# Kernel optimization log

Hardware: AMD Instinct MI355X
Metric: run time of the kernel (lower is better)

The kernel has to match this reference:

```python
import jax, jax.numpy as jnp
import numpy as np

B, N, C, HEADS, P, H, W, TC, ITERS = 2, 4, 128, 8, 4, 96, 96, 64, 3
HD = C // HEADS  # 16
SHIFTS = [(0, 0), (-1, 0), (1, 0), (0, -1), (0, 1)]  # (dx, dy)


def conv1x1(x, w, b):
    # x [B,C,H,W], w [O,C], b [O]
    return jnp.einsum('bchw,oc->bohw', x, w) + b[None, :, None, None]


def grid_sample_bilinear(v, grid):
    # v [M,C,H,W]; grid [M,H,W,2] (x,y) in [-1,1]; align_corners=True, border padding
    M, Cc, Hh, Ww = v.shape
    ix = (grid[..., 0] + 1.0) * 0.5 * (Ww - 1)
    iy = (grid[..., 1] + 1.0) * 0.5 * (Hh - 1)
    x0 = jnp.floor(ix); y0 = jnp.floor(iy)
    wx = (ix - x0)[:, None]; wy = (iy - y0)[:, None]  # [M,1,H,W]
    x0i = jnp.clip(x0, 0, Ww - 1).astype(jnp.int32)
    x1i = jnp.clip(x0 + 1, 0, Ww - 1).astype(jnp.int32)
    y0i = jnp.clip(y0, 0, Hh - 1).astype(jnp.int32)
    y1i = jnp.clip(y0 + 1, 0, Hh - 1).astype(jnp.int32)
    vf = v.reshape(M, Cc, Hh * Ww)
    def gather(yi, xi):
        idx = (yi * Ww + xi).reshape(M, 1, Hh * Ww)
        return jnp.take_along_axis(vf, idx, axis=2).reshape(M, Cc, Hh, Ww)
    return (gather(y0i, x0i) * (1 - wx) * (1 - wy)
            + gather(y0i, x1i) * wx * (1 - wy)
            + gather(y1i, x0i) * (1 - wx) * wy
            + gather(y1i, x1i) * wx * wy)


def gru_cell(x, h, wih, whh, bih, bhh):
    gi = x @ wih.T + bih
    gh = h @ whh.T + bhh
    ir, iz, in_ = jnp.split(gi, 3, axis=-1)
    hr, hz, hn = jnp.split(gh, 3, axis=-1)
    r = jax.nn.sigmoid(ir + hr)
    z = jax.nn.sigmoid(iz + hz)
    n = jnp.tanh(in_ + r * hn)
    return (1.0 - z) * n + z * h


def _correlation_offsets(q, vn):
    # q, vn: [B,HEADS,HD,H,W]
    offset_vals = jnp.asarray(np.array(SHIFTS, dtype=np.float32))  # [5,2] (dx,dy)
    scores = []
    for dx, dy in SHIFTS:
        vs = jnp.roll(vn, shift=(dy, dx), axis=(-2, -1))
        if dy > 0: vs = vs.at[..., :dy, :].set(0.0)
        if dy < 0: vs = vs.at[..., dy:, :].set(0.0)
        if dx > 0: vs = vs.at[..., :, :dx].set(0.0)
        if dx < 0: vs = vs.at[..., :, dx:].set(0.0)
        scores.append((q * vs).sum(axis=2))  # [B,HEADS,H,W]
    best = jnp.argmax(jnp.stack(scores, axis=-1), axis=-1)  # [B,HEADS,H,W]
    bo = offset_vals[best]  # [B,HEADS,H,W,2]
    return jnp.stack([bo[..., 1] * (2.0 / W), bo[..., 0] * (2.0 / H)], axis=-1)


def _forward(query, values, rel_time, time_enc, qw, qb, vw, vb, dww, dwb, pww, pwb,
             wih, whh, bih, bhh, offw, offb, aw, ab, tw, tb, o1w, o1b, o2w, o2b, gate):
    q = conv1x1(query, qw, qb)
    v = conv1x1(values.reshape(B * N, C, H, W), vw, vb).reshape(B, N, C, H, W)
    q_heads = q.reshape(B, HEADS, HD, H, W)
    v_heads = v.reshape(B, N, HEADS, HD, H, W)

    # cnet: depthwise 7x7 -> GELU -> 1x1
    net = jax.lax.conv_general_dilated(query, dww, (1, 1), ((3, 3), (3, 3)),
                                       feature_group_count=C,
                                       dimension_numbers=('NCHW', 'OIHW', 'NCHW'))
    net = jax.nn.gelu(net + dwb[None, :, None, None], approximate=False)
    net = conv1x1(net, pww, pwb)
    net = net.reshape(B, HEADS, HD, H, W).transpose(0, 1, 3, 4, 2).reshape(-1, HD)

    nearest_idx = jnp.argmin(jnp.abs(rel_time), axis=1)  # [B]
    v_nearest = v_heads[jnp.arange(B), nearest_idx]  # [B,HEADS,HD,H,W]

    best_offset = _correlation_offsets(q_heads, v_nearest)  # [B,HEADS,H,W,2]
    curr_offsets = jnp.repeat(best_offset[:, :, :, :, None, :], P, axis=4)
    curr_attn = jnp.zeros((B, HEADS, H, W, N, P), jnp.float32)

    gy, gx = jnp.meshgrid(jnp.linspace(-1.0, 1.0, H), jnp.linspace(-1.0, 1.0, W), indexing='ij')
    base_grid = jnp.stack([gx, gy], axis=-1)  # [H,W,2]

    v_flat = v_nearest.reshape(B * HEADS, HD, H, W)
    for _ in range(ITERS):
        p0 = curr_offsets[..., 0, :]  # [B,HEADS,H,W,2]
        sg = jnp.clip((base_grid[None, None] + p0).reshape(B * HEADS, H, W, 2), -1.0, 1.0)
        sampled = grid_sample_bilinear(v_flat, sg)  # [B*HEADS,HD,H,W]
        sampled = sampled.transpose(0, 2, 3, 1).reshape(-1, HD)
        gru_in = jnp.concatenate([sampled, p0.reshape(-1, 2)], axis=-1)
        net = gru_cell(gru_in, net, wih, whh, bih, bhh)
        d_off = (net @ offw.T + offb).reshape(B, HEADS, H, W, P, 2)
        d_attn = (net @ aw.T + ab).reshape(B, HEADS, H, W, P)
        curr_offsets = curr_offsets + d_off
        curr_attn = curr_attn + d_attn[:, :, :, :, None, :]

    t_bias = (time_enc @ tw.T + tb).transpose(0, 2, 1).reshape(B, HEADS, 1, 1, N, 1)
    final_attn = curr_attn + t_bias
    attn_w = jax.nn.softmax(final_attn.reshape(B, HEADS, H, W, N * P), axis=-1)
    attn_w = attn_w.reshape(B, HEADS, H, W, N, P)

    # deformable sampling over all frames/points, vectorized via vmap
    grids = jnp.clip(base_grid[None, None, :, :, None, :] + curr_offsets, -1.0, 1.0)
    grids = grids.transpose(4, 0, 1, 2, 3, 5).reshape(P, B * HEADS, H, W, 2)
    v_all = v_heads.transpose(1, 0, 2, 3, 4, 5).reshape(N, B * HEADS, HD, H, W)
    samples = jax.vmap(lambda vn: jax.vmap(lambda g: grid_sample_bilinear(vn, g))(grids))(v_all)
    samples = samples.reshape(N, P, B, HEADS, HD, H, W)
    out = jnp.einsum('npbhcyx,bhyxnp->bhcyx', samples, attn_w).reshape(B, C, H, W)

    out = conv1x1(out, o1w, o1b)
    out = jax.nn.gelu(out, approximate=False)
    out = conv1x1(out, o2w, o2b) * jax.nn.sigmoid(gate)

    af = attn_w.reshape(B, HEADS, H, W, N * P)
    entropy = -(af * jnp.log(af + 1e-8)).sum(axis=-1).mean(axis=1, keepdims=True)
    max_ent = float(np.log(N * P))
    confidence = 1.0 - jnp.clip(entropy / (max_ent + 1e-8), 0.0, 1.0)
    return out, confidence, entropy


def setup_inputs():
    key = jax.random.key(0)
    ks = jax.random.split(key, 30)
    def nrm(k, shape, s=1.0):
        return jax.random.normal(k, shape, jnp.float32) * s
    s = 0.05
    return {
        'query': nrm(ks[0], (B, C, H, W)),
        'values': nrm(ks[1], (B, N, C, H, W)),
        'rel_time': nrm(ks[2], (B, N)),
        'time_enc': nrm(ks[3], (B, N, TC)),
        'qw': nrm(ks[4], (C, C), s), 'qb': nrm(ks[5], (C,), s),
        'vw': nrm(ks[6], (C, C), s), 'vb': nrm(ks[7], (C,), s),
        'dww': nrm(ks[8], (C, 1, 7, 7), s), 'dwb': nrm(ks[9], (C,), s),
        'pww': nrm(ks[10], (C, C), s), 'pwb': nrm(ks[11], (C,), s),
        'wih': nrm(ks[12], (3 * HD, HD + 2), s), 'whh': nrm(ks[13], (3 * HD, HD), s),
        'bih': nrm(ks[14], (3 * HD,), s), 'bhh': nrm(ks[15], (3 * HD,), s),
        'offw': nrm(ks[16], (P * 2, HD), s), 'offb': nrm(ks[17], (P * 2,), s),
        'aw': nrm(ks[18], (P, HD), s), 'ab': nrm(ks[19], (P,), s),
        'tw': nrm(ks[20], (HEADS, TC), s), 'tb': nrm(ks[21], (HEADS,), s),
        'o1w': nrm(ks[22], (C, C), s), 'o1b': nrm(ks[23], (C,), s),
        'o2w': nrm(ks[24], (C, C), s), 'o2b': nrm(ks[25], (C,), s),
        'gate': nrm(ks[26], (1, C, 1, 1), s),
    }


def reference(query, values, rel_time, time_enc, qw, qb, vw, vb, dww, dwb, pww, pwb,
              wih, whh, bih, bhh, offw, offb, aw, ab, tw, tb, o1w, o1b, o2w, o2b, gate):
    return _forward(query, values, rel_time, time_enc, qw, qb, vw, vb, dww, dwb, pww, pwb,
                    wih, whh, bih, bhh, offw, offb, aw, ab, tw, tb, o1w, o1b, o2w, o2b, gate)
```

## Files before the change

kernel.cpp:

```cpp
#include <hip/hip_runtime.h>
#include <hip/hip_bf16.h>

typedef unsigned short u16;
typedef unsigned int   u32;

constexpr int kHW = 9216;
constexpr int kM  = 147456;

__device__ __forceinline__ float gelu_f(float v){ return 0.5f*v*(1.0f+erff(v*0.70710678118654752f)); }
__device__ __forceinline__ float sigm_f(float v){ return 1.0f/(1.0f+expf(-v)); }
__device__ __forceinline__ u16 f2bf(float f){
  u32 x = __float_as_uint(f);
  return (u16)((x + 0x7fffu + ((x>>16)&1u)) >> 16);
}
__device__ __forceinline__ int nearest_n(const float* __restrict__ relt, int b){
  int nidx = 0; float bv = fabsf(relt[b*4]);
  for (int n = 1; n < 4; ++n){ float a = fabsf(relt[b*4+n]); if (a < bv){ bv=a; nidx=n; } }
  return nidx;
}

struct Bilin { int i00,i10,i01,i11; float w00,w10,w01,w11; };

__device__ __forceinline__ Bilin make_bilin(int x, int y, float ox, float oy){
  float gx = fmaf((float)x, 2.0f/95.0f, -1.0f);
  float gy = fmaf((float)y, 2.0f/95.0f, -1.0f);
  float sgx = fminf(fmaxf(gx+ox,-1.0f),1.0f);
  float sgy = fminf(fmaxf(gy+oy,-1.0f),1.0f);
  float ix = (sgx+1.0f)*0.5f*95.0f;
  float iy = (sgy+1.0f)*0.5f*95.0f;
  float x0f = floorf(ix), y0f = floorf(iy);
  float wx = ix-x0f, wy = iy-y0f;
  int x0 = min(max((int)x0f,0),95), y0 = min(max((int)y0f,0),95);
  int x1 = min(x0+1,95), y1 = min(y0+1,95);
  Bilin b;
  b.i00=(y0*96+x0)*16; b.i10=(y0*96+x1)*16; b.i01=(y1*96+x0)*16; b.i11=(y1*96+x1)*16;
  float iwx=1.0f-wx, iwy=1.0f-wy;
  b.w00=iwx*iwy; b.w10=wx*iwy; b.w01=iwx*wy; b.w11=wx*wy;
  return b;
}

__device__ __forceinline__ void sample16(const float* __restrict__ vp, const Bilin& bl, float* __restrict__ o){
  const float4* p00 = (const float4*)(vp + bl.i00);
  const float4* p10 = (const float4*)(vp + bl.i10);
  const float4* p01 = (const float4*)(vp + bl.i01);
  const float4* p11 = (const float4*)(vp + bl.i11);
  #pragma unroll
  for (int g = 0; g < 4; ++g){
    float4 a=p00[g], b=p10[g], c=p01[g], d=p11[g];
    o[g*4+0] = a.x*bl.w00 + b.x*bl.w10 + c.x*bl.w01 + d.x*bl.w11;
    o[g*4+1] = a.y*bl.w00 + b.y*bl.w10 + c.y*bl.w01 + d.y*bl.w11;
    o[g*4+2] = a.z*bl.w00 + b.z*bl.w10 + c.z*bl.w01 + d.z*bl.w11;
    o[g*4+3] = a.w*bl.w00 + b.w*bl.w10 + c.w*bl.w01 + d.w*bl.w11;
  }
}

__global__ __launch_bounds__(256) void prep_k(const float* __restrict__ qw, const float* __restrict__ vw,
    const float* __restrict__ pww, const float* __restrict__ o1w, const float* __restrict__ o2w,
    float* __restrict__ wt)
{
  const float* src = (blockIdx.y==0)?qw:(blockIdx.y==1)?vw:(blockIdx.y==2)?pww:(blockIdx.y==3)?o1w:o2w;
  float* d = wt + blockIdx.y*16384;
  int i = blockIdx.x*256 + threadIdx.x;
  int o = i & 127, c = i >> 7;
  d[i] = src[o*128 + c];
}

__global__ __launch_bounds__(256, 3) void gemm_qvp_k(
    const float* __restrict__ query, const float* __restrict__ values, const float* __restrict__ dwbuf,
    const float* __restrict__ wtb,
    const float* __restrict__ qb2, const float* __restrict__ vb2, const float* __restrict__ pwb2,
    float* __restrict__ qbuf, float* __restrict__ netb,
    float* __restrict__ vf32n, u16* __restrict__ vb16, const float* __restrict__ relt)
{
  __shared__ __align__(16) float a_s[16*132];
  __shared__ __align__(16) float b_s[16*132];
  const int tid = threadIdx.x;
  const int tx = tid & 15, ty = tid >> 4;
  const int iy = blockIdx.y;
  const float* inp; const float* wt; const float* bias; int img; int mode;
  if (iy < 2)       { inp = query;  wt = wtb;         bias = qb2;  img = iy;      mode = 0; }
  else if (iy < 10) { inp = values; wt = wtb + 16384; bias = vb2;  img = iy - 2;  mode = 1; }
  else              { inp = dwbuf;  wt = wtb + 32768; bias = pwb2; img = iy - 10; mode = 2; }
  const int px0 = blockIdx.x * 128;
  const int sr = tid >> 4;
  const int sc = (tid & 15) * 8;

  float acc[64];
  #pragma unroll
  for (int oj = 0; oj < 8; ++oj) {
    float bv = bias[tx*8+oj];
    #pragma unroll
    for (int pi = 0; pi < 8; ++pi) acc[pi*8+oj] = bv;
  }

  for (int kc = 0; kc < 8; ++kc) {
    const int k0 = kc*16;
    { const float4* g = (const float4*)(wt + (k0+sr)*128 + sc);
      float4 v0 = g[0], v1 = g[1];
      *(float4*)&b_s[sr*132+sc] = v0; *(float4*)&b_s[sr*132+sc+4] = v1; }
    { const float4* g = (const float4*)(inp + (size_t)(img*128 + k0 + sr)*kHW + px0 + sc);
      float4 v0 = g[0], v1 = g[1];
      *(float4*)&a_s[sr*132+sc] = v0; *(float4*)&a_s[sr*132+sc+4] = v1; }
    __syncthreads();
    #pragma unroll
    for (int k = 0; k < 16; ++k) {
      float4 b0 = *(const float4*)&b_s[k*132 + tx*8];
      float4 b1 = *(const float4*)&b_s[k*132 + tx*8 + 4];
      float4 a0 = *(const float4*)&a_s[k*132 + ty*8];
      float4 a1 = *(const float4*)&a_s[k*132 + ty*8 + 4];
      float av[8] = {a0.x,a0.y,a0.z,a0.w,a1.x,a1.y,a1.z,a1.w};
      float bv[8] = {b0.x,b0.y,b0.z,b0.w,b1.x,b1.y,b1.z,b1.w};
      #pragma unroll
      for (int pi = 0; pi < 8; ++pi)
        #pragma unroll
        for (int oj = 0; oj < 8; ++oj)
          acc[pi*8+oj] = fmaf(av[pi], bv[oj], acc[pi*8+oj]);
    }
    __syncthreads();
  }

  const int head = tx >> 1, hd0 = (tx & 1)*8;
  if (mode == 1) {
    const int b = img >> 2, n = img & 3;
    const int nidx = nearest_n(relt, b);
    #pragma unroll
    for (int pi = 0; pi < 8; ++pi) {
      const int px = px0 + ty*8 + pi;
      u16* d16 = vb16 + ((size_t)(img*8 + head)*kHW + px)*16 + hd0;
      uint4 packed;
      packed.x = (u32)f2bf(acc[pi*8+0]) | ((u32)f2bf(acc[pi*8+1])<<16);
      packed.y = (u32)f2bf(acc[pi*8+2]) | ((u32)f2bf(acc[pi*8+3])<<16);
      packed.z = (u32)f2bf(acc[pi*8+4]) | ((u32)f2bf(acc[pi*8+5])<<16);
      packed.w = (u32)f2bf(acc[pi*8+6]) | ((u32)f2bf(acc[pi*8+7])<<16);
      *(uint4*)d16 = packed;
      if (n == nidx) {
        float* dst = vf32n + ((size_t)(b*8 + head)*kHW + px)*16 + hd0;
        float4 t0 = {acc[pi*8+0],acc[pi*8+1],acc[pi*8+2],acc[pi*8+3]};
        float4 t1 = {acc[pi*8+4],acc[pi*8+5],acc[pi*8+6],acc[pi*8+7]};
        *(float4*)dst = t0; *(float4*)(dst+4) = t1;
      }
    }
  } else {
    float* outf = (mode == 0) ? qbuf : netb;
    #pragma unroll
    for (int pi = 0; pi < 8; ++pi) {
      const int px = px0 + ty*8 + pi;
      float* dst = outf + ((size_t)(img*8 + head)*kHW + px)*16 + hd0;
      float4 t0 = {acc[pi*8+0],acc[pi*8+1],acc[pi*8+2],acc[pi*8+3]};
      float4 t1 = {acc[pi*8+4],acc[pi*8+5],acc[pi*8+6],acc[pi*8+7]};
      *(float4*)dst = t0; *(float4*)(dst+4) = t1;
    }
  }
}

__global__ __launch_bounds__(256) void o1o2_k(const u16* __restrict__ oat,
    const float* __restrict__ wt1, const float* __restrict__ o1b,
    const float* __restrict__ wt2, const float* __restrict__ o2b,
    const float* __restrict__ gate, float* __restrict__ out)
{
  __shared__ __align__(16) float a_s[16*132];
  __shared__ __align__(16) float b_s[16*132];
  __shared__ __align__(16) float mid[128*132];
  const int tid = threadIdx.x;
  const int tx = tid & 15, ty = tid >> 4;
  const int img = blockIdx.y;
  const int px0 = blockIdx.x * 128;
  const int sr = tid >> 4;
  const int sc = (tid & 15) * 8;

  float acc[64];
  #pragma unroll
  for (int oj = 0; oj < 8; ++oj) {
    float bv = o1b[tx*8+oj];
    #pragma unroll
    for (int pi = 0; pi < 8; ++pi) acc[pi*8+oj] = bv;
  }
  for (int kc = 0; kc < 8; ++kc) {
    const int k0 = kc*16;
    { const float4* g = (const float4*)(wt1 + (k0+sr)*128 + sc);
      float4 v0 = g[0], v1 = g[1];
      *(float4*)&b_s[sr*132+sc] = v0; *(float4*)&b_s[sr*132+sc+4] = v1; }
    { const int px = tid >> 1, hd0 = (tid & 1)*8;
      uint4 raw = *(const uint4*)(oat + ((size_t)(img*8 + kc)*kHW + px0 + px)*16 + hd0);
      u32 w[4] = {raw.x, raw.y, raw.z, raw.w};
      #pragma unroll
      for (int gi = 0; gi < 4; ++gi) {
        a_s[(hd0+gi*2+0)*132+px] = __uint_as_float(w[gi]<<16);
        a_s[(hd0+gi*2+1)*132+px] = __uint_as_float(w[gi]&0xffff0000u);
      }
    }
    __syncthreads();
    #pragma unroll
    for (int k = 0; k < 16; ++k) {
      float4 b0 = *(const float4*)&b_s[k*132 + tx*8];
      float4 b1 = *(const float4*)&b_s[k*132 + tx*8 + 4];
      float4 a0 = *(const float4*)&a_s[k*132 + ty*8];
      float4 a1 = *(const float4*)&a_s[k*132 + ty*8 + 4];
      float av[8] = {a0.x,a0.y,a0.z,a0.w,a1.x,a1.y,a1.z,a1.w};
      float bv[8] = {b0.x,b0.y,b0.z,b0.w,b1.x,b1.y,b1.z,b1.w};
      #pragma unroll
      for (int pi = 0; pi < 8; ++pi)
        #pragma unroll
        for (int oj = 0; oj < 8; ++oj)
          acc[pi*8+oj] = fmaf(av[pi], bv[oj], acc[pi*8+oj]);
    }
    __syncthreads();
  }
  #pragma unroll
  for (int oj = 0; oj < 8; ++oj)
    #pragma unroll
    for (int pi = 0; pi < 8; ++pi)
      mid[(tx*8+oj)*132 + ty*8+pi] = gelu_f(acc[pi*8+oj]);
  __syncthreads();

  #pragma unroll
  for (int oj = 0; oj < 8; ++oj) {
    float bv = o2b[tx*8+oj];
    #pragma unroll
    for (int pi = 0; pi < 8; ++pi) acc[pi*8+oj] = bv;
  }
  for (int kc = 0; kc < 8; ++kc) {
    const int k0 = kc*16;
    { const float4* g = (const float4*)(wt2 + (k0+sr)*128 + sc);
      float4 v0 = g[0], v1 = g[1];
      *(float4*)&b_s[sr*132+sc] = v0; *(float4*)&b_s[sr*132+sc+4] = v1; }
    __syncthreads();
    #pragma unroll
    for (int k = 0; k < 16; ++k) {
      float4 b0 = *(const float4*)&b_s[k*132 + tx*8];
      float4 b1 = *(const float4*)&b_s[k*132 + tx*8 + 4];
      float4 a0 = *(const float4*)&mid[(k0+k)*132 + ty*8];
      float4 a1 = *(const float4*)&mid[(k0+k)*132 + ty*8 + 4];
      float av[8] = {a0.x,a0.y,a0.z,a0.w,a1.x,a1.y,a1.z,a1.w};
      float bv[8] = {b0.x,b0.y,b0.z,b0.w,b1.x,b1.y,b1.z,b1.w};
      #pragma unroll
      for (int pi = 0; pi < 8; ++pi)
        #pragma unroll
        for (int oj = 0; oj < 8; ++oj)
          acc[pi*8+oj] = fmaf(av[pi], bv[oj], acc[pi*8+oj]);
    }
    __syncthreads();
  }
  #pragma unroll
  for (int oj = 0; oj < 8; ++oj) {
    const int o = tx*8 + oj;
    float* dst = out + (size_t)(img*128 + o)*kHW + px0 + ty*8;
    float sg = sigm_f(gate[o]);
    float v[8];
    #pragma unroll
    for (int pi = 0; pi < 8; ++pi) v[pi] = acc[pi*8+oj] * sg;
    float4 t0 = {v[0],v[1],v[2],v[3]};
    float4 t1 = {v[4],v[5],v[6],v[7]};
    *(float4*)dst = t0; *(float4*)(dst+4) = t1;
  }
}

__global__ __launch_bounds__(256) void dw_k(const float* __restrict__ q, const float* __restrict__ dww,
    const float* __restrict__ dwb, float* __restrict__ outf)
{
  int idx = blockIdx.x*256 + threadIdx.x;
  int px = idx % kHW;
  int bc = idx / kHW;
  int c = bc & 127;
  int x = px % 96, y = px / 96;
  float s = dwb[c];
  const float* qb = q + (size_t)bc*kHW;
  #pragma unroll
  for (int ky = 0; ky < 7; ++ky) {
    int yy = y + ky - 3;
    if (yy < 0 || yy > 95) continue;
    #pragma unroll
    for (int kx = 0; kx < 7; ++kx) {
      int xx = x + kx - 3;
      if (xx < 0 || xx > 95) continue;
      s = fmaf(qb[yy*96+xx], dww[c*49 + ky*7 + kx], s);
    }
  }
  outf[idx] = gelu_f(s);
}

__global__ void tb_k(const float* __restrict__ te, const float* __restrict__ tw,
                     const float* __restrict__ tbias, float* __restrict__ tbb)
{
  int i = threadIdx.x;
  if (i >= 64) return;
  int b = i >> 5, h = (i >> 2) & 7, n = i & 3;
  float s = tbias[h];
  for (int tc = 0; tc < 64; ++tc) s = fmaf(te[(b*4+n)*64 + tc], tw[h*64+tc], s);
  tbb[(b*8+h)*4 + n] = s;
}

__global__ __launch_bounds__(256) void fused_k(
    const float* __restrict__ qb, const float* __restrict__ vf32, const u16* __restrict__ vb16,
    const float* __restrict__ netb, const float* __restrict__ relt,
    const float* __restrict__ wih, const float* __restrict__ whh,
    const float* __restrict__ bihp, const float* __restrict__ bhhp,
    const float* __restrict__ offw, const float* __restrict__ offbp,
    const float* __restrict__ aw, const float* __restrict__ abp,
    const float* __restrict__ tbb,
    u16* __restrict__ outattn16, float* __restrict__ entb)
{
  __shared__ __align__(16) float s_wih[48*20];
  __shared__ __align__(16) float s_whh[48*16];
  __shared__ __align__(16) float s_offw[8*16];
  __shared__ __align__(16) float s_aw[4*16];
  __shared__ float s_bih[48], s_bhh[48], s_offb[8], s_ab[4];
  const int tid = threadIdx.x;
  for (int i = tid; i < 960; i += 256){ int g = i/20, k = i%20; s_wih[i] = (k<18)? wih[g*18+k] : 0.0f; }
  for (int i = tid; i < 768; i += 256) s_whh[i] = whh[i];
  if (tid < 128) s_offw[tid] = offw[tid];
  if (tid < 64)  s_aw[tid]  = aw[tid];
  if (tid < 48){ s_bih[tid] = bihp[tid]; s_bhh[tid] = bhhp[tid]; }
  if (tid < 8)   s_offb[tid] = offbp[tid];
  if (tid < 4)   s_ab[tid]  = abp[tid];

  const int vblk = (blockIdx.x & 7)*72 + (blockIdx.x >> 3);
  const int item = vblk*256 + tid;
  const int yx = item % kHW; const int bh = item / kHW;
  const int b = bh >> 3, head = bh & 7;
  const int x = yx % 96, y = yx / 96;
  const float* vp = vf32 + (size_t)(b*8 + head)*kM;

  float off_[8], attn_[4];
  {
    float qv[16];
    { const float4* q4 = (const float4*)(qb + (size_t)bh*kM + yx*16);
      #pragma unroll
      for (int g = 0; g < 4; ++g){ float4 t = q4[g]; qv[g*4]=t.x; qv[g*4+1]=t.y; qv[g*4+2]=t.z; qv[g*4+3]=t.w; } }
    const int sdx[5] = {0,-1,1,0,0};
    const int sdy[5] = {0,0,0,-1,1};
    float4 tv[5][4]; bool valid[5];
    #pragma unroll
    for (int s5 = 0; s5 < 5; ++s5) {
      int sy = y - sdy[s5], sx = x - sdx[s5];
      valid[s5] = (sy >= 0 && sy < 96 && sx >= 0 && sx < 96);
      int syc = min(max(sy,0),95), sxc = min(max(sx,0),95);
      const float4* tp = (const float4*)(vp + (syc*96+sxc)*16);
      tv[s5][0] = tp[0]; tv[s5][1] = tp[1]; tv[s5][2] = tp[2]; tv[s5][3] = tp[3];
    }
    double bsc = 0.0; int best = 0;
    #pragma unroll
    for (int s5 = 0; s5 < 5; ++s5) {
      double sc = 0.0;
      if (valid[s5]) {
        const float* tp = (const float*)&tv[s5][0];
        #pragma unroll
        for (int hd = 0; hd < 16; ++hd) sc += (double)qv[hd]*(double)tp[hd];
      }
      if (s5 == 0) { bsc = sc; best = 0; }
      else if (sc > bsc) { bsc = sc; best = s5; }
    }
    const float STEP = 2.0f/96.0f;
    float ox = 0.f, oy = 0.f;
    if (best == 3) ox = -STEP; else if (best == 4) ox = STEP;
    if (best == 1) oy = -STEP; else if (best == 2) oy = STEP;
    #pragma unroll
    for (int p = 0; p < 4; ++p) { off_[2*p] = ox; off_[2*p+1] = oy; attn_[p] = 0.0f; }
  }

  float h[16];
  { const float4* n4 = (const float4*)(netb + (size_t)item*16);
    #pragma unroll
    for (int g = 0; g < 4; ++g){ float4 t = n4[g]; h[g*4]=t.x; h[g*4+1]=t.y; h[g*4+2]=t.z; h[g*4+3]=t.w; } }

  __syncthreads();

  for (int it = 0; it < 3; ++it) {
    const float p0x = off_[0];
    const float p0y = off_[1];
    Bilin bl = make_bilin(x, y, p0x, p0y);
    float xv[20];
    sample16(vp, bl, xv);
    xv[16] = p0x; xv[17] = p0y; xv[18] = 0.f; xv[19] = 0.f;

    float hn[16];
    #pragma unroll 2
    for (int j = 0; j < 16; ++j) {
      float g0 = s_bih[j], g1 = s_bih[16+j], g2 = s_bih[32+j];
      const float4* w0r = (const float4*)&s_wih[j*20];
      const float4* w1r = (const float4*)&s_wih[(16+j)*20];
      const float4* w2r = (const float4*)&s_wih[(32+j)*20];
      #pragma unroll
      for (int q4 = 0; q4 < 5; ++q4) {
        float4 w0 = w0r[q4], w1 = w1r[q4], w2 = w2r[q4];
        float a0 = xv[q4*4+0], a1 = xv[q4*4+1], a2 = xv[q4*4+2], a3 = xv[q4*4+3];
        g0 = fmaf(a0,w0.x,g0); g0 = fmaf(a1,w0.y,g0); g0 = fmaf(a2,w0.z,g0); g0 = fmaf(a3,w0.w,g0);
        g1 = fmaf(a0,w1.x,g1); g1 = fmaf(a1,w1.y,g1); g1 = fmaf(a2,w1.z,g1); g1 = fmaf(a3,w1.w,g1);
        g2 = fmaf(a0,w2.x,g2); g2 = fmaf(a1,w2.y,g2); g2 = fmaf(a2,w2.z,g2); g2 = fmaf(a3,w2.w,g2);
      }
      float t0 = s_bhh[j], t1 = s_bhh[16+j], t2 = s_bhh[32+j];
      const float4* h0r = (const float4*)&s_whh[j*16];
      const float4* h1r = (const float4*)&s_whh[(16+j)*16];
      const float4* h2r = (const float4*)&s_whh[(32+j)*16];
      #pragma unroll
      for (int q4 = 0; q4 < 4; ++q4) {
        float4 w0 = h0r[q4], w1 = h1r[q4], w2 = h2r[q4];
        float a0 = h[q4*4+0], a1 = h[q4*4+1], a2 = h[q4*4+2], a3 = h[q4*4+3];
        t0 = fmaf(a0,w0.x,t0); t0 = fmaf(a1,w0.y,t0); t0 = fmaf(a2,w0.z,t0); t0 = fmaf(a3,w0.w,t0);
        t1 = fmaf(a0,w1.x,t1); t1 = fmaf(a1,w1.y,t1); t1 = fmaf(a2,w1.z,t1); t1 = fmaf(a3,w1.w,t1);
        t2 = fmaf(a0,w2.x,t2); t2 = fmaf(a1,w2.y,t2); t2 = fmaf(a2,w2.z,t2); t2 = fmaf(a3,w2.w,t2);
      }
      float r = sigm_f(g0 + t0);
      float z = sigm_f(g1 + t1);
      float nn = tanhf(fmaf(r, t2, g2));
      hn[j] = fmaf(z, h[j], (1.0f - z)*nn);
    }
    #pragma unroll
    for (int j = 0; j < 16; ++j) h[j] = hn[j];

    #pragma unroll
    for (int d = 0; d < 8; ++d) {
      const float4* wr = (const float4*)&s_offw[d*16];
      float s = s_offb[d];
      #pragma unroll
      for (int q4 = 0; q4 < 4; ++q4) {
        float4 w4 = wr[q4];
        s = fmaf(h[q4*4+0], w4.x, s); s = fmaf(h[q4*4+1], w4.y, s);
        s = fmaf(h[q4*4+2], w4.z, s); s = fmaf(h[q4*4+3], w4.w, s);
      }
      off_[d] += s;
    }
    #pragma unroll
    for (int p = 0; p < 4; ++p) {
      const float4* wr = (const float4*)&s_aw[p*16];
      float s = s_ab[p];
      #pragma unroll
      for (int q4 = 0; q4 < 4; ++q4) {
        float4 w4 = wr[q4];
        s = fmaf(h[q4*4+0], w4.x, s); s = fmaf(h[q4*4+1], w4.y, s);
        s = fmaf(h[q4*4+2], w4.z, s); s = fmaf(h[q4*4+3], w4.w, s);
      }
      attn_[p] += s;
    }
  }

  float lg[16];
  #pragma unroll
  for (int n = 0; n < 4; ++n) {
    float tv2 = tbb[(b*8+head)*4 + n];
    #pragma unroll
    for (int p = 0; p < 4; ++p) lg[n*4+p] = attn_[p] + tv2;
  }
  float mx = lg[0];
  #pragma unroll
  for (int i = 1; i < 16; ++i) mx = fmaxf(mx, lg[i]);
  float es = 0.f;
  #pragma unroll
  for (int i = 0; i < 16; ++i){ lg[i] = expf(lg[i]-mx); es += lg[i]; }
  float inv = 1.0f/es;
  float ent = 0.f;
  #pragma unroll
  for (int i = 0; i < 16; ++i){ lg[i] *= inv; ent -= lg[i]*logf(lg[i] + 1e-8f); }
  entb[item] = ent;

  float acc[16];
  #pragma unroll
  for (int j = 0; j < 16; ++j) acc[j] = 0.f;
  #pragma unroll
  for (int p = 0; p < 4; ++p) {
    Bilin bl = make_bilin(x, y, off_[2*p], off_[2*p+1]);
    uint4 raw[4][8];
    #pragma unroll
    for (int n = 0; n < 4; ++n) {
      const u16* vpn = vb16 + (size_t)((b*4+n)*8 + head)*kM;
      raw[n][0] = *(const uint4*)(vpn + bl.i00); raw[n][1] = *(const uint4*)(vpn + bl.i00 + 8);
      raw[n][2] = *(const uint4*)(vpn + bl.i10); raw[n][3] = *(const uint4*)(vpn + bl.i10 + 8);
      raw[n][4] = *(const uint4*)(vpn + bl.i01); raw[n][5] = *(const uint4*)(vpn + bl.i01 + 8);
      raw[n][6] = *(const uint4*)(vpn + bl.i11); raw[n][7] = *(const uint4*)(vpn + bl.i11 + 8);
    }
    #pragma unroll
    for (int n = 0; n < 4; ++n) {
      u32 aw2[8] = {raw[n][0].x,raw[n][0].y,raw[n][0].z,raw[n][0].w, raw[n][1].x,raw[n][1].y,raw[n][1].z,raw[n][1].w};
      u32 bw2[8] = {raw[n][2].x,raw[n][2].y,raw[n][2].z,raw[n][2].w, raw[n][3].x,raw[n][3].y,raw[n][3].z,raw[n][3].w};
      u32 cw2[8] = {raw[n][4].x,raw[n][4].y,raw[n][4].z,raw[n][4].w, raw[n][5].x,raw[n][5].y,raw[n][5].z,raw[n][5].w};
      u32 dw2[8] = {raw[n][6].x,raw[n][6].y,raw[n][6].z,raw[n][6].w, raw[n][7].x,raw[n][7].y,raw[n][7].z,raw[n][7].w};
      float wnp = lg[n*4+p];
      #pragma unroll
      for (int g = 0; g < 8; ++g){
        float alo = __uint_as_float(aw2[g]<<16), ahi = __uint_as_float(aw2[g]&0xffff0000u);
        float blo = __uint_as_float(bw2[g]<<16), bhi = __uint_as_float(bw2[g]&0xffff0000u);
        float clo = __uint_as_float(cw2[g]<<16), chi = __uint_as_float(cw2[g]&0xffff0000u);
        float dlo = __uint_as_float(dw2[g]<<16), dhi = __uint_as_float(dw2[g]&0xffff0000u);
        float s0 = alo*bl.w00 + blo*bl.w10 + clo*bl.w01 + dlo*bl.w11;
        float s1 = ahi*bl.w00 + bhi*bl.w10 + chi*bl.w01 + dhi*bl.w11;
        acc[g*2+0] = fmaf(wnp, s0, acc[g*2+0]);
        acc[g*2+1] = fmaf(wnp, s1, acc[g*2+1]);
      }
    }
  }
  uint4 pk0, pk1;
  pk0.x = (u32)f2bf(acc[0])  | ((u32)f2bf(acc[1])<<16);
  pk0.y = (u32)f2bf(acc[2])  | ((u32)f2bf(acc[3])<<16);
  pk0.z = (u32)f2bf(acc[4])  | ((u32)f2bf(acc[5])<<16);
  pk0.w = (u32)f2bf(acc[6])  | ((u32)f2bf(acc[7])<<16);
  pk1.x = (u32)f2bf(acc[8])  | ((u32)f2bf(acc[9])<<16);
  pk1.y = (u32)f2bf(acc[10]) | ((u32)f2bf(acc[11])<<16);
  pk1.z = (u32)f2bf(acc[12]) | ((u32)f2bf(acc[13])<<16);
  pk1.w = (u32)f2bf(acc[14]) | ((u32)f2bf(acc[15])<<16);
  *(uint4*)(outattn16 + (size_t)item*16)     = pk0;
  *(uint4*)(outattn16 + (size_t)item*16 + 8) = pk1;
}

__global__ __launch_bounds__(256) void ent_k(const float* __restrict__ entb, float* __restrict__ outf)
{
  int idx = blockIdx.x*256 + threadIdx.x;
  int b = idx / kHW, yx = idx % kHW;
  float s = 0.f;
  #pragma unroll
  for (int h8 = 0; h8 < 8; ++h8) s += entb[(b*8+h8)*kHW + yx];
  s *= 0.125f;
  float conf = 1.0f - fminf(fmaxf(s / (2.772588722239781f + 1e-8f), 0.0f), 1.0f);
  outf[2359296 + idx]         = conf;
  outf[2359296 + 18432 + idx] = s;
}

extern "C" void kernel_launch(void* const* d_in, const int* in_sizes, int n_in,
                              void* d_out, int out_size, void* d_ws, size_t ws_size,
                              hipStream_t stream)
{
  const float* query  = (const float*)d_in[0];
  const float* values = (const float*)d_in[1];
  const float* relt   = (const float*)d_in[2];
  const float* time_enc = (const float*)d_in[3];
  const float* qw  = (const float*)d_in[4];
  const float* qb  = (const float*)d_in[5];
  const float* vw  = (const float*)d_in[6];
  const float* vb  = (const float*)d_in[7];
  const float* dww = (const float*)d_in[8];
  const float* dwb = (const float*)d_in[9];
  const float* pww = (const float*)d_in[10];
  const float* pwb = (const float*)d_in[11];
  const float* wih = (const float*)d_in[12];
  const float* whh = (const float*)d_in[13];
  const float* bih = (const float*)d_in[14];
  const float* bhh = (const float*)d_in[15];
  const float* offw = (const float*)d_in[16];
  const float* offb = (const float*)d_in[17];
  const float* aw  = (const float*)d_in[18];
  const float* ab  = (const float*)d_in[19];
  const float* tw  = (const float*)d_in[20];
  const float* tb  = (const float*)d_in[21];
  const float* o1w = (const float*)d_in[22];
  const float* o1b = (const float*)d_in[23];
  const float* o2w = (const float*)d_in[24];
  const float* o2b = (const float*)d_in[25];
  const float* gate = (const float*)d_in[26];
  float* out = (float*)d_out;
  float* ws = (float*)d_ws;

  u16*   vb16   = (u16*)ws;
  float* vf32n  = ws + 4718592;
  float* qbuf   = ws + 7077888;
  float* netb   = ws + 9437184;
  float* dwbuf  = ws + 11796480;
  u16*   oat16  = (u16*)dwbuf;
  float* entbf  = ws + 14155776;
  float* tbbuf  = ws + 14303232;
  float* wtbuf  = ws + 14303360;
  if (ws_size < 14385280ull * 4ull) return;

  float* wt_o1 = wtbuf + 49152;
  float* wt_o2 = wtbuf + 65536;

  dim3 blk(256,1,1);
  prep_k<<<dim3(64,5,1), blk, 0, stream>>>(qw, vw, pww, o1w, o2w, wtbuf);
  dw_k<<<dim3(9216,1,1), blk, 0, stream>>>(query, dww, dwb, dwbuf);
  gemm_qvp_k<<<dim3(72,12,1), blk, 0, stream>>>(query, values, dwbuf, wtbuf,
                                                qb, vb, pwb, qbuf, netb, vf32n, vb16, relt);
  tb_k<<<dim3(1,1,1), dim3(64,1,1), 0, stream>>>(time_enc, tw, tb, tbbuf);
  fused_k<<<dim3(576,1,1), blk, 0, stream>>>(qbuf, vf32n, vb16, netb, relt,
                                             wih, whh, bih, bhh, offw, offb, aw, ab,
                                             tbbuf, oat16, entbf);
  ent_k<<<dim3(72,1,1), blk, 0, stream>>>(entbf, out);
  o1o2_k<<<dim3(72,2,1), blk, 0, stream>>>(oat16, wt_o1, o1b, wt_o2, o2b, gate, out);
}
```

Measured before the change: 434.8 us.

## Halve o1o2 pixel tile and read GRU weights directly from global memory

Measured after the change: 445.5 us. +2.5%, slower.

```diff
diff --git a/kernel.cpp b/kernel.cpp
--- a/kernel.cpp
+++ b/kernel.cpp
@@ -158,48 +158,44 @@
     const float* __restrict__ wt2, const float* __restrict__ o2b,
     const float* __restrict__ gate, float* __restrict__ out)
 {
-  __shared__ __align__(16) float a_s[16*132];
+  __shared__ __align__(16) float a_s[16*68];
   __shared__ __align__(16) float b_s[16*132];
-  __shared__ __align__(16) float mid[128*132];
+  __shared__ __align__(16) float mid[128*68];
   const int tid = threadIdx.x;
   const int tx = tid & 15, ty = tid >> 4;
   const int img = blockIdx.y;
-  const int px0 = blockIdx.x * 128;
+  const int px0 = blockIdx.x * 64;
   const int sr = tid >> 4;
   const int sc = (tid & 15) * 8;
 
-  float acc[64];
+  float acc[32];
   #pragma unroll
   for (int oj = 0; oj < 8; ++oj) {
     float bv = o1b[tx*8+oj];
     #pragma unroll
-    for (int pi = 0; pi < 8; ++pi) acc[pi*8+oj] = bv;
+    for (int pi = 0; pi < 4; ++pi) acc[pi*8+oj] = bv;
   }
   for (int kc = 0; kc < 8; ++kc) {
     const int k0 = kc*16;
     { const float4* g = (const float4*)(wt1 + (k0+sr)*128 + sc);
       float4 v0 = g[0], v1 = g[1];
       *(float4*)&b_s[sr*132+sc] = v0; *(float4*)&b_s[sr*132+sc+4] = v1; }
-    { const int px = tid >> 1, hd0 = (tid & 1)*8;
-      uint4 raw = *(const uint4*)(oat + ((size_t)(img*8 + kc)*kHW + px0 + px)*16 + hd0);
-      u32 w[4] = {raw.x, raw.y, raw.z, raw.w};
-      #pragma unroll
-      for (int gi = 0; gi < 4; ++gi) {
-        a_s[(hd0+gi*2+0)*132+px] = __uint_as_float(w[gi]<<16);
-        a_s[(hd0+gi*2+1)*132+px] = __uint_as_float(w[gi]&0xffff0000u);
-      }
-    }
+    { const int px = tid & 63, hd0 = (tid >> 6) * 4;
+      uint2 raw = *(const uint2*)(oat + ((size_t)(img*8 + kc)*kHW + px0 + px)*16 + hd0);
+      a_s[(hd0+0)*68+px] = __uint_as_float(raw.x<<16);
+      a_s[(hd0+1)*68+px] = __uint_as_float(raw.x&0xffff0000u);
+      a_s[(hd0+2)*68+px] = __uint_as_float(raw.y<<16);
+      a_s[(hd0+3)*68+px] = __uint_as_float(raw.y&0xffff0000u); }
     __syncthreads();
     #pragma unroll
     for (int k = 0; k < 16; ++k) {
       float4 b0 = *(const float4*)&b_s[k*132 + tx*8];
       float4 b1 = *(const float4*)&b_s[k*132 + tx*8 + 4];
-      float4 a0 = *(const float4*)&a_s[k*132 + ty*8];
-      float4 a1 = *(const float4*)&a_s[k*132 + ty*8 + 4];
-      float av[8] = {a0.x,a0.y,a0.z,a0.w,a1.x,a1.y,a1.z,a1.w};
+      float4 a0 = *(const float4*)&a_s[k*68 + ty*4];
+      float av[4] = {a0.x,a0.y,a0.z,a0.w};
       float bv[8] = {b0.x,b0.y,b0.z,b0.w,b1.x,b1.y,b1.z,b1.w};
       #pragma unroll
-      for (int pi = 0; pi < 8; ++pi)
+      for (int pi = 0; pi < 4; ++pi)
         #pragma unroll
         for (int oj = 0; oj < 8; ++oj)
           acc[pi*8+oj] = fmaf(av[pi], bv[oj], acc[pi*8+oj]);
@@ -209,15 +205,15 @@
   #pragma unroll
   for (int oj = 0; oj < 8; ++oj)
     #pragma unroll
-    for (int pi = 0; pi < 8; ++pi)
-      mid[(tx*8+oj)*132 + ty*8+pi] = gelu_f(acc[pi*8+oj]);
+    for (int pi = 0; pi < 4; ++pi)
+      mid[(tx*8+oj)*68 + ty*4+pi] = gelu_f(acc[pi*8+oj]);
   __syncthreads();
 
   #pragma unroll
   for (int oj = 0; oj < 8; ++oj) {
     float bv = o2b[tx*8+oj];
     #pragma unroll
-    for (int pi = 0; pi < 8; ++pi) acc[pi*8+oj] = bv;
+    for (int pi = 0; pi < 4; ++pi) acc[pi*8+oj] = bv;
   }
   for (int kc = 0; kc < 8; ++kc) {
     const int k0 = kc*16;
@@ -229,12 +225,11 @@
     for (int k = 0; k < 16; ++k) {
       float4 b0 = *(const float4*)&b_s[k*132 + tx*8];
       float4 b1 = *(const float4*)&b_s[k*132 + tx*8 + 4];
-      float4 a0 = *(const float4*)&mid[(k0+k)*132 + ty*8];
-      float4 a1 = *(const float4*)&mid[(k0+k)*132 + ty*8 + 4];
-      float av[8] = {a0.x,a0.y,a0.z,a0.w,a1.x,a1.y,a1.z,a1.w};
+      float4 a0 = *(const float4*)&mid[(k0+k)*68 + ty*4];
+      float av[4] = {a0.x,a0.y,a0.z,a0.w};
       float bv[8] = {b0.x,b0.y,b0.z,b0.w,b1.x,b1.y,b1.z,b1.w};
       #pragma unroll
-      for (int pi = 0; pi < 8; ++pi)
+      for (int pi = 0; pi < 4; ++pi)
         #pragma unroll
         for (int oj = 0; oj < 8; ++oj)
           acc[pi*8+oj] = fmaf(av[pi], bv[oj], acc[pi*8+oj]);
@@ -244,14 +239,10 @@
   #pragma unroll
   for (int oj = 0; oj < 8; ++oj) {
     const int o = tx*8 + oj;
-    float* dst = out + (size_t)(img*128 + o)*kHW + px0 + ty*8;
+    float* dst = out + (size_t)(img*128 + o)*kHW + px0 + ty*4;
     float sg = sigm_f(gate[o]);
-    float v[8];
-    #pragma unroll
-    for (int pi = 0; pi < 8; ++pi) v[pi] = acc[pi*8+oj] * sg;
-    float4 t0 = {v[0],v[1],v[2],v[3]};
-    float4 t1 = {v[4],v[5],v[6],v[7]};
-    *(float4*)dst = t0; *(float4*)(dst+4) = t1;
+    float4 t0 = {acc[0*8+oj]*sg, acc[1*8+oj]*sg, acc[2*8+oj]*sg, acc[3*8+oj]*sg};
+    *(float4*)dst = t0;
   }
 }
 
@@ -300,20 +291,7 @@
     const float* __restrict__ tbb,
     u16* __restrict__ outattn16, float* __restrict__ entb)
 {
-  __shared__ __align__(16) float s_wih[48*20];
-  __shared__ __align__(16) float s_whh[48*16];
-  __shared__ __align__(16) float s_offw[8*16];
-  __shared__ __align__(16) float s_aw[4*16];
-  __shared__ float s_bih[48], s_bhh[48], s_offb[8], s_ab[4];
   const int tid = threadIdx.x;
-  for (int i = tid; i < 960; i += 256){ int g = i/20, k = i%20; s_wih[i] = (k<18)? wih[g*18+k] : 0.0f; }
-  for (int i = tid; i < 768; i += 256) s_whh[i] = whh[i];
-  if (tid < 128) s_offw[tid] = offw[tid];
-  if (tid < 64)  s_aw[tid]  = aw[tid];
-  if (tid < 48){ s_bih[tid] = bihp[tid]; s_bhh[tid] = bhhp[tid]; }
-  if (tid < 8)   s_offb[tid] = offbp[tid];
-  if (tid < 4)   s_ab[tid]  = abp[tid];
-
   const int vblk = (blockIdx.x & 7)*72 + (blockIdx.x >> 3);
   const int item = vblk*256 + tid;
   const int yx = item % kHW; const int bh = item / kHW;
@@ -363,42 +341,38 @@
     #pragma unroll
     for (int g = 0; g < 4; ++g){ float4 t = n4[g]; h[g*4]=t.x; h[g*4+1]=t.y; h[g*4+2]=t.z; h[g*4+3]=t.w; } }
 
-  __syncthreads();
-
   for (int it = 0; it < 3; ++it) {
     const float p0x = off_[0];
     const float p0y = off_[1];
     Bilin bl = make_bilin(x, y, p0x, p0y);
-    float xv[20];
+    float xv[18];
     sample16(vp, bl, xv);
-    xv[16] = p0x; xv[17] = p0y; xv[18] = 0.f; xv[19] = 0.f;
+    xv[16] = p0x; xv[17] = p0y;
 
     float hn[16];
     #pragma unroll 2
     for (int j = 0; j < 16; ++j) {
-      float g0 = s_bih[j], g1 = s_bih[16+j], g2 = s_bih[32+j];
-      const float4* w0r = (const float4*)&s_wih[j*20];
-      const float4* w1r = (const float4*)&s_wih[(16+j)*20];
-      const float4* w2r = (const float4*)&s_wih[(32+j)*20];
-      #pragma unroll
-      for (int q4 = 0; q4 < 5; ++q4) {
-        float4 w0 = w0r[q4], w1 = w1r[q4], w2 = w2r[q4];
-        float a0 = xv[q4*4+0], a1 = xv[q4*4+1], a2 = xv[q4*4+2], a3 = xv[q4*4+3];
-        g0 = fmaf(a0,w0.x,g0); g0 = fmaf(a1,w0.y,g0); g0 = fmaf(a2,w0.z,g0); g0 = fmaf(a3,w0.w,g0);
-        g1 = fmaf(a0,w1.x,g1); g1 = fmaf(a1,w1.y,g1); g1 = fmaf(a2,w1.z,g1); g1 = fmaf(a3,w1.w,g1);
-        g2 = fmaf(a0,w2.x,g2); g2 = fmaf(a1,w2.y,g2); g2 = fmaf(a2,w2.z,g2); g2 = fmaf(a3,w2.w,g2);
+      float g0 = bihp[j], g1 = bihp[16+j], g2 = bihp[32+j];
+      const float* w0 = wih + j*18;
+      const float* w1 = wih + (16+j)*18;
+      const float* w2 = wih + (32+j)*18;
+      #pragma unroll
+      for (int k = 0; k < 18; ++k) {
+        float a = xv[k];
+        g0 = fmaf(a, w0[k], g0);
+        g1 = fmaf(a, w1[k], g1);
+        g2 = fmaf(a, w2[k], g2);
       }
-      float t0 = s_bhh[j], t1 = s_bhh[16+j], t2 = s_bhh[32+j];
-      const float4* h0r = (const float4*)&s_whh[j*16];
-      const float4* h1r = (const float4*)&s_whh[(16+j)*16];
-      const float4* h2r = (const float4*)&s_whh[(32+j)*16];
-      #pragma unroll
-      for (int q4 = 0; q4 < 4; ++q4) {
-        float4 w0 = h0r[q4], w1 = h1r[q4], w2 = h2r[q4];
-        float a0 = h[q4*4+0], a1 = h[q4*4+1], a2 = h[q4*4+2], a3 = h[q4*4+3];
-        t0 = fmaf(a0,w0.x,t0); t0 = fmaf(a1,w0.y,t0); t0 = fmaf(a2,w0.z,t0); t0 = fmaf(a3,w0.w,t0);
-        t1 = fmaf(a0,w1.x,t1); t1 = fmaf(a1,w1.y,t1); t1 = fmaf(a2,w1.z,t1); t1 = fmaf(a3,w1.w,t1);
-        t2 = fmaf(a0,w2.x,t2); t2 = fmaf(a1,w2.y,t2); t2 = fmaf(a2,w2.z,t2); t2 = fmaf(a3,w2.w,t2);
+      float t0 = bhhp[j], t1 = bhhp[16+j], t2 = bhhp[32+j];
+      const float* v0 = whh + j*16;
+      const float* v1 = whh + (16+j)*16;
+      const float* v2 = whh + (32+j)*16;
+      #pragma unroll
+      for (int k = 0; k < 16; ++k) {
+        float a = h[k];
+        t0 = fmaf(a, v0[k], t0);
+        t1 = fmaf(a, v1[k], t1);
+        t2 = fmaf(a, v2[k], t2);
       }
       float r = sigm_f(g0 + t0);
       float z = sigm_f(g1 + t1);
@@ -410,26 +384,18 @@
 
     #pragma unroll
     for (int d = 0; d < 8; ++d) {
-      const float4* wr = (const float4*)&s_offw[d*16];
-      float s = s_offb[d];
-      #pragma unroll
-      for (int q4 = 0; q4 < 4; ++q4) {
-        float4 w4 = wr[q4];
-        s = fmaf(h[q4*4+0], w4.x, s); s = fmaf(h[q4*4+1], w4.y, s);
-        s = fmaf(h[q4*4+2], w4.z, s); s = fmaf(h[q4*4+3], w4.w, s);
-      }
+      const float* wr = offw + d*16;
+      float s = offbp[d];
+      #pragma unroll
+      for (int k = 0; k < 16; ++k) s = fmaf(h[k], wr[k], s);
       off_[d] += s;
     }
     #pragma unroll
     for (int p = 0; p < 4; ++p) {
-      const float4* wr = (const float4*)&s_aw[p*16];
-      float s = s_ab[p];
-      #pragma unroll
-      for (int q4 = 0; q4 < 4; ++q4) {
-        float4 w4 = wr[q4];
-        s = fmaf(h[q4*4+0], w4.x, s); s = fmaf(h[q4*4+1], w4.y, s);
-        s = fmaf(h[q4*4+2], w4.z, s); s = fmaf(h[q4*4+3], w4.w, s);
-      }
+      const float* wr = aw + p*16;
+      float s = abp[p];
+      #pragma unroll
+      for (int k = 0; k < 16; ++k) s = fmaf(h[k], wr[k], s);
       attn_[p] += s;
     }
   }
@@ -572,5 +538,5 @@
                                              wih, whh, bih, bhh, offw, offb, aw, ab,
                                              tbbuf, oat16, entbf);
   ent_k<<<dim3(72,1,1), blk, 0, stream>>>(entbf, out);
-  o1o2_k<<<dim3(72,2,1), blk, 0, stream>>>(oat16, wt_o1, o1b, wt_o2, o2b, gate, out);
-}
+  o1o2_k<<<dim3(144,2,1), blk, 0, stream>>>(oat16, wt_o1, o1b, wt_o2, o2b, gate, out);
+}
```

## Merge small launches and shrink output-MLP tile to raise block count

Applied to the files above, without the earlier changes.

Result: faster. 423.6 us (-2.6%).

```diff
diff --git a/kernel.cpp b/kernel.cpp
--- a/kernel.cpp
+++ b/kernel.cpp
@@ -54,15 +54,49 @@
   }
 }
 
-__global__ __launch_bounds__(256) void prep_k(const float* __restrict__ qw, const float* __restrict__ vw,
-    const float* __restrict__ pww, const float* __restrict__ o1w, const float* __restrict__ o2w,
-    float* __restrict__ wt)
+__global__ __launch_bounds__(256) void pre_k(
+    const float* __restrict__ query, const float* __restrict__ dww, const float* __restrict__ dwb,
+    float* __restrict__ dwbuf,
+    const float* __restrict__ qw, const float* __restrict__ vw, const float* __restrict__ pww,
+    const float* __restrict__ o1w, const float* __restrict__ o2w, float* __restrict__ wt,
+    const float* __restrict__ te, const float* __restrict__ tw, const float* __restrict__ tbias,
+    float* __restrict__ tbb)
 {
-  const float* src = (blockIdx.y==0)?qw:(blockIdx.y==1)?vw:(blockIdx.y==2)?pww:(blockIdx.y==3)?o1w:o2w;
-  float* d = wt + blockIdx.y*16384;
-  int i = blockIdx.x*256 + threadIdx.x;
-  int o = i & 127, c = i >> 7;
-  d[i] = src[o*128 + c];
+  const int bid = blockIdx.x;
+  const int tid = threadIdx.x;
+  if (bid < 9216) {
+    int idx = bid*256 + tid;
+    int px = idx % kHW;
+    int bc = idx / kHW;
+    int c = bc & 127;
+    int x = px % 96, y = px / 96;
+    float s = dwb[c];
+    const float* qb = query + (size_t)bc*kHW;
+    #pragma unroll
+    for (int ky = 0; ky < 7; ++ky) {
+      int yy = y + ky - 3;
+      if (yy < 0 || yy > 95) continue;
+      #pragma unroll
+      for (int kx = 0; kx < 7; ++kx) {
+        int xx = x + kx - 3;
+        if (xx < 0 || xx > 95) continue;
+        s = fmaf(qb[yy*96+xx], dww[c*49 + ky*7 + kx], s);
+      }
+    }
+    dwbuf[idx] = gelu_f(s);
+  } else if (bid < 9536) {
+    int i = (bid - 9216)*256 + tid;
+    int m = i >> 14, r = i & 16383;
+    const float* src = (m==0)?qw:(m==1)?vw:(m==2)?pww:(m==3)?o1w:o2w;
+    int o = r & 127, c = r >> 7;
+    wt[m*16384 + r] = src[o*128 + c];
+  } else {
+    if (tid >= 64) return;
+    int b = tid >> 5, h = (tid >> 2) & 7, n = tid & 3;
+    float s = tbias[h];
+    for (int tc = 0; tc < 64; ++tc) s = fmaf(te[(b*4+n)*64 + tc], tw[h*64+tc], s);
+    tbb[(b*8+h)*4 + n] = s;
+  }
 }
 
 __global__ __launch_bounds__(256, 3) void gemm_qvp_k(
@@ -151,143 +185,6 @@
       *(float4*)dst = t0; *(float4*)(dst+4) = t1;
     }
   }
-}
-
-__global__ __launch_bounds__(256) void o1o2_k(const u16* __restrict__ oat,
-    const float* __restrict__ wt1, const float* __restrict__ o1b,
-    const float* __restrict__ wt2, const float* __restrict__ o2b,
-    const float* __restrict__ gate, float* __restrict__ out)
-{
-  __shared__ __align__(16) float a_s[16*132];
-  __shared__ __align__(16) float b_s[16*132];
-  __shared__ __align__(16) float mid[128*132];
-  const int tid = threadIdx.x;
-  const int tx = tid & 15, ty = tid >> 4;
-  const int img = blockIdx.y;
-  const int px0 = blockIdx.x * 128;
-  const int sr = tid >> 4;
-  const int sc = (tid & 15) * 8;
-
-  float acc[64];
-  #pragma unroll
-  for (int oj = 0; oj < 8; ++oj) {
-    float bv = o1b[tx*8+oj];
-    #pragma unroll
-    for (int pi = 0; pi < 8; ++pi) acc[pi*8+oj] = bv;
-  }
-  for (int kc = 0; kc < 8; ++kc) {
-    const int k0 = kc*16;
-    { const float4* g = (const float4*)(wt1 + (k0+sr)*128 + sc);
-      float4 v0 = g[0], v1 = g[1];
-      *(float4*)&b_s[sr*132+sc] = v0; *(float4*)&b_s[sr*132+sc+4] = v1; }
-    { const int px = tid >> 1, hd0 = (tid & 1)*8;
-      uint4 raw = *(const uint4*)(oat + ((size_t)(img*8 + kc)*kHW + px0 + px)*16 + hd0);
-      u32 w[4] = {raw.x, raw.y, raw.z, raw.w};
-      #pragma unroll
-      for (int gi = 0; gi < 4; ++gi) {
-        a_s[(hd0+gi*2+0)*132+px] = __uint_as_float(w[gi]<<16);
-        a_s[(hd0+gi*2+1)*132+px] = __uint_as_float(w[gi]&0xffff0000u);
-      }
-    }
-    __syncthreads();
-    #pragma unroll
-    for (int k = 0; k < 16; ++k) {
-      float4 b0 = *(const float4*)&b_s[k*132 + tx*8];
-      float4 b1 = *(const float4*)&b_s[k*132 + tx*8 + 4];
-      float4 a0 = *(const float4*)&a_s[k*132 + ty*8];
-      float4 a1 = *(const float4*)&a_s[k*132 + ty*8 + 4];
-      float av[8] = {a0.x,a0.y,a0.z,a0.w,a1.x,a1.y,a1.z,a1.w};
-      float bv[8] = {b0.x,b0.y,b0.z,b0.w,b1.x,b1.y,b1.z,b1.w};
-      #pragma unroll
-      for (int pi = 0; pi < 8; ++pi)
-        #pragma unroll
-        for (int oj = 0; oj < 8; ++oj)
-          acc[pi*8+oj] = fmaf(av[pi], bv[oj], acc[pi*8+oj]);
-    }
-    __syncthreads();
-  }
-  #pragma unroll
-  for (int oj = 0; oj < 8; ++oj)
-    #pragma unroll
-    for (int pi = 0; pi < 8; ++pi)
-      mid[(tx*8+oj)*132 + ty*8+pi] = gelu_f(acc[pi*8+oj]);
-  __syncthreads();
-
-  #pragma unroll
-  for (int oj = 0; oj < 8; ++oj) {
-    float bv = o2b[tx*8+oj];
-    #pragma unroll
-    for (int pi = 0; pi < 8; ++pi) acc[pi*8+oj] = bv;
-  }
-  for (int kc = 0; kc < 8; ++kc) {
-    const int k0 = kc*16;
-    { const float4* g = (const float4*)(wt2 + (k0+sr)*128 + sc);
-      float4 v0 = g[0], v1 = g[1];
-      *(float4*)&b_s[sr*132+sc] = v0; *(float4*)&b_s[sr*132+sc+4] = v1; }
-    __syncthreads();
-    #pragma unroll
-    for (int k = 0; k < 16; ++k) {
-      float4 b0 = *(const float4*)&b_s[k*132 + tx*8];
-      float4 b1 = *(const float4*)&b_s[k*132 + tx*8 + 4];
-      float4 a0 = *(const float4*)&mid[(k0+k)*132 + ty*8];
-      float4 a1 = *(const float4*)&mid[(k0+k)*132 + ty*8 + 4];
-      float av[8] = {a0.x,a0.y,a0.z,a0.w,a1.x,a1.y,a1.z,a1.w};
-      float bv[8] = {b0.x,b0.y,b0.z,b0.w,b1.x,b1.y,b1.z,b1.w};
-      #pragma unroll
-      for (int pi = 0; pi < 8; ++pi)
-        #pragma unroll
-        for (int oj = 0; oj < 8; ++oj)
-          acc[pi*8+oj] = fmaf(av[pi], bv[oj], acc[pi*8+oj]);
-    }
-    __syncthreads();
-  }
-  #pragma unroll
-  for (int oj = 0; oj < 8; ++oj) {
-    const int o = tx*8 + oj;
-    float* dst = out + (size_t)(img*128 + o)*kHW + px0 + ty*8;
-    float sg = sigm_f(gate[o]);
-    float v[8];
-    #pragma unroll
-    for (int pi = 0; pi < 8; ++pi) v[pi] = acc[pi*8+oj] * sg;
-    float4 t0 = {v[0],v[1],v[2],v[3]};
-    float4 t1 = {v[4],v[5],v[6],v[7]};
-    *(float4*)dst = t0; *(float4*)(dst+4) = t1;
-  }
-}
-
-__global__ __launch_bounds__(256) void dw_k(const float* __restrict__ q, const float* __restrict__ dww,
-    const float* __restrict__ dwb, float* __restrict__ outf)
-{
-  int idx = blockIdx.x*256 + threadIdx.x;
-  int px = idx % kHW;
-  int bc = idx / kHW;
-  int c = bc & 127;
-  int x = px % 96, y = px / 96;
-  float s = dwb[c];
-  const float* qb = q + (size_t)bc*kHW;
-  #pragma unroll
-  for (int ky = 0; ky < 7; ++ky) {
-    int yy = y + ky - 3;
-    if (yy < 0 || yy > 95) continue;
-    #pragma unroll
-    for (int kx = 0; kx < 7; ++kx) {
-      int xx = x + kx - 3;
-      if (xx < 0 || xx > 95) continue;
-      s = fmaf(qb[yy*96+xx], dww[c*49 + ky*7 + kx], s);
-    }
-  }
-  outf[idx] = gelu_f(s);
-}
-
-__global__ void tb_k(const float* __restrict__ te, const float* __restrict__ tw,
-                     const float* __restrict__ tbias, float* __restrict__ tbb)
-{
-  int i = threadIdx.x;
-  if (i >= 64) return;
-  int b = i >> 5, h = (i >> 2) & 7, n = i & 3;
-  float s = tbias[h];
-  for (int tc = 0; tc < 64; ++tc) s = fmaf(te[(b*4+n)*64 + tc], tw[h*64+tc], s);
-  tbb[(b*8+h)*4 + n] = s;
 }
 
 __global__ __launch_bounds__(256) void fused_k(
@@ -501,17 +398,110 @@
   *(uint4*)(outattn16 + (size_t)item*16 + 8) = pk1;
 }
 
-__global__ __launch_bounds__(256) void ent_k(const float* __restrict__ entb, float* __restrict__ outf)
+__global__ __launch_bounds__(256) void tail_k(const u16* __restrict__ oat,
+    const float* __restrict__ wt1, const float* __restrict__ o1b,
+    const float* __restrict__ wt2, const float* __restrict__ o2b,
+    const float* __restrict__ gate, const float* __restrict__ entb, float* __restrict__ out)
 {
-  int idx = blockIdx.x*256 + threadIdx.x;
-  int b = idx / kHW, yx = idx % kHW;
-  float s = 0.f;
-  #pragma unroll
-  for (int h8 = 0; h8 < 8; ++h8) s += entb[(b*8+h8)*kHW + yx];
-  s *= 0.125f;
-  float conf = 1.0f - fminf(fmaxf(s / (2.772588722239781f + 1e-8f), 0.0f), 1.0f);
-  outf[2359296 + idx]         = conf;
-  outf[2359296 + 18432 + idx] = s;
+  __shared__ __align__(16) float a_s[16*68];
+  __shared__ __align__(16) float b_s[16*132];
+  __shared__ __align__(16) float mid[128*68];
+  const int tid = threadIdx.x;
+  if (blockIdx.y == 2) {
+    if (blockIdx.x >= 72) return;
+    int idx = blockIdx.x*256 + tid;
+    int b = idx / kHW, yx = idx % kHW;
+    float s = 0.f;
+    #pragma unroll
+    for (int h8 = 0; h8 < 8; ++h8) s += entb[(b*8+h8)*kHW + yx];
+    s *= 0.125f;
+    float conf = 1.0f - fminf(fmaxf(s / (2.772588722239781f + 1e-8f), 0.0f), 1.0f);
+    out[2359296 + idx]         = conf;
+    out[2359296 + 18432 + idx] = s;
+    return;
+  }
+  const int tx = tid & 15, ty = tid >> 4;
+  const int img = blockIdx.y;
+  const int px0 = blockIdx.x * 64;
+  const int sr = tid >> 4;
+  const int sc = (tid & 15) * 8;
+
+  float acc[32];
+  #pragma unroll
+  for (int oj = 0; oj < 8; ++oj) {
+    float bv = o1b[tx*8+oj];
+    #pragma unroll
+    for (int pi = 0; pi < 4; ++pi) acc[pi*8+oj] = bv;
+  }
+  for (int kc = 0; kc < 8; ++kc) {
+    const int k0 = kc*16;
+    { const float4* g = (const float4*)(wt1 + (k0+sr)*128 + sc);
+      float4 v0 = g[0], v1 = g[1];
+      *(float4*)&b_s[sr*132+sc] = v0; *(float4*)&b_s[sr*132+sc+4] = v1; }
+    { const int px = tid & 63, hd0 = (tid >> 6) * 4;
+      uint2 raw = *(const uint2*)(oat + ((size_t)(img*8 + kc)*kHW + px0 + px)*16 + hd0);
+      a_s[(hd0+0)*68+px] = __uint_as_float(raw.x<<16);
+      a_s[(hd0+1)*68+px] = __uint_as_float(raw.x&0xffff0000u);
+      a_s[(hd0+2)*68+px] = __uint_as_float(raw.y<<16);
+      a_s[(hd0+3)*68+px] = __uint_as_float(raw.y&0xffff0000u); }
+    __syncthreads();
+    #pragma unroll
+    for (int k = 0; k < 16; ++k) {
+      float4 b0 = *(const float4*)&b_s[k*132 + tx*8];
+      float4 b1 = *(const float4*)&b_s[k*132 + tx*8 + 4];
+      float4 a0 = *(const float4*)&a_s[k*68 + ty*4];
+      float av[4] = {a0.x,a0.y,a0.z,a0.w};
+      float bv[8] = {b0.x,b0.y,b0.z,b0.w,b1.x,b1.y,b1.z,b1.w};
+      #pragma unroll
+      for (int pi = 0; pi < 4; ++pi)
+        #pragma unroll
+        for (int oj = 0; oj < 8; ++oj)
+          acc[pi*8+oj] = fmaf(av[pi], bv[oj], acc[pi*8+oj]);
+    }
+    __syncthreads();
+  }
+  #pragma unroll
+  for (int oj = 0; oj < 8; ++oj)
+    #pragma unroll
+    for (int pi = 0; pi < 4; ++pi)
+      mid[(tx*8+oj)*68 + ty*4+pi] = gelu_f(acc[pi*8+oj]);
+  __syncthreads();
+
+  #pragma unroll
+  for (int oj = 0; oj < 8; ++oj) {
+    float bv = o2b[tx*8+oj];
+    #pragma unroll
+    for (int pi = 0; pi < 4; ++pi) acc[pi*8+oj] = bv;
+  }
+  for (int kc = 0; kc < 8; ++kc) {
+    const int k0 = kc*16;
+    { const float4* g = (const float4*)(wt2 + (k0+sr)*128 + sc);
+      float4 v0 = g[0], v1 = g[1];
+      *(float4*)&b_s[sr*132+sc] = v0; *(float4*)&b_s[sr*132+sc+4] = v1; }
+    __syncthreads();
+    #pragma unroll
+    for (int k = 0; k < 16; ++k) {
+      float4 b0 = *(const float4*)&b_s[k*132 + tx*8];
+      float4 b1 = *(const float4*)&b_s[k*132 + tx*8 + 4];
+      float4 a0 = *(const float4*)&mid[(k0+k)*68 + ty*4];
+      float av[4] = {a0.x,a0.y,a0.z,a0.w};
+      float bv[8] = {b0.x,b0.y,b0.z,b0.w,b1.x,b1.y,b1.z,b1.w};
+      #pragma unroll
+      for (int pi = 0; pi < 4; ++pi)
+        #pragma unroll
+        for (int oj = 0; oj < 8; ++oj)
+          acc[pi*8+oj] = fmaf(av[pi], bv[oj], acc[pi*8+oj]);
+    }
+    __syncthreads();
+  }
+  #pragma unroll
+  for (int oj = 0; oj < 8; ++oj) {
+    const int o = tx*8 + oj;
+    float* dst = out + (size_t)(img*128 + o)*kHW + px0 + ty*4;
+    float sg = sigm_f(gate[o]);
+    float4 t0 = {acc[0*8+oj]*sg, acc[1*8+oj]*sg, acc[2*8+oj]*sg, acc[3*8+oj]*sg};
+    *(float4*)dst = t0;
+  }
 }
 
 extern "C" void kernel_launch(void* const* d_in, const int* in_sizes, int n_in,
@@ -563,14 +553,13 @@
   float* wt_o2 = wtbuf + 65536;
 
   dim3 blk(256,1,1);
-  prep_k<<<dim3(64,5,1), blk, 0, stream>>>(qw, vw, pww, o1w, o2w, wtbuf);
-  dw_k<<<dim3(9216,1,1), blk, 0, stream>>>(query, dww, dwb, dwbuf);
+  pre_k<<<dim3(9537,1,1), blk, 0, stream>>>(query, dww, dwb, dwbuf,
+                                            qw, vw, pww, o1w, o2w, wtbuf,
+                                            time_enc, tw, tb, tbbuf);
   gemm_qvp_k<<<dim3(72,12,1), blk, 0, stream>>>(query, values, dwbuf, wtbuf,
                                                 qb, vb, pwb, qbuf, netb, vf32n, vb16, relt);
-  tb_k<<<dim3(1,1,1), dim3(64,1,1), 0, stream>>>(time_enc, tw, tb, tbbuf);
   fused_k<<<dim3(576,1,1), blk, 0, stream>>>(qbuf, vf32n, vb16, netb, relt,
                                              wih, whh, bih, bhh, offw, offb, aw, ab,
                                              tbbuf, oat16, entbf);
-  ent_k<<<dim3(72,1,1), blk, 0, stream>>>(entbf, out);
-  o1o2_k<<<dim3(72,2,1), blk, 0, stream>>>(oat16, wt_o1, o1b, wt_o2, o2b, gate, out);
-}
+  tail_k<<<dim3(144,3,1), blk, 0, stream>>>(oat16, wt_o1, o1b, wt_o2, o2b, gate, entbf, out);
+}
```
